# Optimization experiments

Measured on AMD Instinct MI355X. Metric: run time of the kernel, lower is better.

Reference implementation:

```python
import jax, jax.numpy as jnp
import numpy as np
from jax import lax

B, C, H, W = 8, 128, 128, 128
HEADS = 16
HEAD_C = C // HEADS  # 8
SLOPE = 0.2
EPS = 1e-12


def _conv(x, w, b, padding, groups=1):
    # x: [B,C,H,W], w: [O,I/groups,kh,kw]
    y = lax.conv_general_dilated(
        x, w, window_strides=(1, 1), padding=padding,
        dimension_numbers=("NCHW", "OIHW", "NCHW"),
        feature_group_count=groups)
    return y + b[None, :, None, None]


def _conv_block(x, conv1_w, conv1_b, conv2_w, conv2_b, dw_w, dw_b, sc_w, sc_b):
    h = _conv(x, conv1_w, conv1_b, ((1, 1), (1, 1)))            # 3x3, zero pad
    h = jnp.where(h >= 0, h, SLOPE * h)                          # LeakyReLU
    h = _conv(h, conv2_w, conv2_b, ((0, 0), (0, 0)))             # 1x1
    hp = jnp.pad(h, ((0, 0), (0, 0), (1, 1), (1, 1)), mode="reflect")
    h = _conv(hp, dw_w, dw_b, ((0, 0), (0, 0)), groups=C)        # depthwise 3x3, reflect pad
    h = jnp.where(h >= 0, h, SLOPE * h)
    sc = _conv(x, sc_w, sc_b, ((0, 0), (0, 0)))                  # 1x1 shortcut
    return h + sc


def setup_inputs() -> dict:
    key = jax.random.key(0)
    ks = jax.random.split(key, 10)
    s = 0.05
    return {
        "x1": jax.random.normal(ks[0], (B, C, H, W), jnp.float32),
        "x2": jax.random.normal(ks[1], (B, C, H, W), jnp.float32),
        "temperature": jnp.ones((HEADS, 1, 1), jnp.float32),
        "conv1_w": jax.random.normal(ks[2], (C, C, 3, 3), jnp.float32) * s,
        "conv1_b": jnp.zeros((C,), jnp.float32),
        "conv2_w": jax.random.normal(ks[3], (C, C, 1, 1), jnp.float32) * s,
        "conv2_b": jnp.zeros((C,), jnp.float32),
        "dw_w": jax.random.normal(ks[4], (C, 1, 3, 3), jnp.float32) * s,
        "dw_b": jnp.zeros((C,), jnp.float32),
        "sc_w": jax.random.normal(ks[5], (C, C, 1, 1), jnp.float32) * s,
        "sc_b": jnp.zeros((C,), jnp.float32),
    }


def reference(x1, x2, temperature, conv1_w, conv1_b, conv2_w, conv2_b,
              dw_w, dw_b, sc_w, sc_b):
    b, c, h, w = x2.shape
    # b (head c) h w -> b head c (h w)
    qk = x1.reshape(b, HEADS, HEAD_C, h * w)
    v = x2.reshape(b, HEADS, HEAD_C, h * w)
    # L2-normalize over spatial dim (F.normalize, eps=1e-12)
    norm = jnp.sqrt(jnp.sum(qk * qk, axis=-1, keepdims=True))
    qn = qk / jnp.maximum(norm, EPS)
    # channel attention: [b, head, c, c]
    attn = jnp.einsum("bhcn,bhdn->bhcd", qn, qn) * temperature
    attn = jax.nn.softmax(attn, axis=-1)
    out = jnp.einsum("bhcd,bhdn->bhcn", attn, v)
    out = out.reshape(b, c, h, w)
    out = _conv_block(out, conv1_w, conv1_b, conv2_w, conv2_b,
                      dw_w, dw_b, sc_w, sc_b)
    return out + x1
```

## Files before the change

### kernel.cpp

```cpp
#include <hip/hip_runtime.h>
#include <hip/hip_bf16.h>

typedef __attribute__((ext_vector_type(8))) short short8;
typedef __attribute__((ext_vector_type(4))) float f32x4;

#define NB 8
#define NC 128
#define NHW 128
#define NSP (NHW*NHW)
#define SLOPE 0.2f
#define EPSN 1e-12f
#define PADW 130

static __device__ __forceinline__ unsigned short f2bf(float f) {
    __hip_bfloat16 h = __float2bfloat16(f);
    return *reinterpret_cast<unsigned short*>(&h);
}
static __device__ __forceinline__ float bf2f(__hip_bfloat16 h) {
    return __bfloat162float(h);
}

__global__ void prep_all(const float* __restrict__ c1w, const float* __restrict__ c2w,
                         const float* __restrict__ scw,
                         __hip_bfloat16* __restrict__ wb1, __hip_bfloat16* __restrict__ wb2,
                         __hip_bfloat16* __restrict__ wbsc, __hip_bfloat16* __restrict__ yt2) {
    int idx = blockIdx.x * 256 + threadIdx.x;
    if (idx < 147456) {
        int kw = idx % 3; int t = idx / 3;
        int kh = t % 3;   t /= 3;
        int i  = t % 128; int o = t / 128;
        int tap = kh * 3 + kw;
        int half = i >> 6, icc = (i >> 5) & 1, lk = (i >> 3) & 3, j = i & 7;
        int wn = o >> 6, c = (o >> 4) & 3, l15 = o & 15;
        int lane = lk * 16 + l15;
        size_t chunk = (size_t)tap * 32 + half * 16 + wn * 8 + icc * 4 + c;
        wb1[chunk * 512 + lane * 8 + j] = __float2bfloat16(c1w[idx]);
    } else if (idx < 180224) {
        int i2 = idx - 147456;
        const float* src = (i2 < 16384) ? c2w : scw;
        __hip_bfloat16* dst = (i2 < 16384) ? wb2 : wbsc;
        int e = i2 & 16383;
        int i = e & 127, o = e >> 7;
        int kk = i >> 5, lk = (i >> 3) & 3, j = i & 7;
        int wn = o >> 6, c = (o >> 4) & 3, l15 = o & 15;
        int lane = lk * 16 + l15;
        size_t chunk = ((size_t)(wn * 4 + kk) * 4 + c);
        dst[chunk * 512 + lane * 8 + j] = __float2bfloat16(src[e]);
    } else if (idx < 184352) {
        int t = idx - 180224;
        int b = t / 516, s = t % 516;
        int row, col;
        if (s < 130)      { row = 0;           col = s; }
        else if (s < 260) { row = 129;         col = s - 130; }
        else if (s < 388) { row = s - 260 + 1; col = 0; }
        else              { row = s - 388 + 1; col = 129; }
        uint4* dst = reinterpret_cast<uint4*>(yt2 + ((size_t)(b * PADW + row) * PADW + col) * 128);
        uint4 z = make_uint4(0u, 0u, 0u, 0u);
#pragma unroll
        for (int i = 0; i < 16; ++i) dst[i] = z;
    }
}

__global__ __launch_bounds__(256) void gram_part(const float* __restrict__ x1,
                                                 float* __restrict__ Gp) {
    int bh = blockIdx.x & 127;
    int q  = blockIdx.x >> 7;
    const float* base = x1 + (size_t)bh * 8 * NSP + q * 4096;
    float acc[8][8];
#pragma unroll
    for (int c = 0; c < 8; c++)
#pragma unroll
        for (int d = 0; d < 8; d++) acc[c][d] = 0.f;

    for (int n = threadIdx.x; n < 4096; n += 256) {
        float v[8];
#pragma unroll
        for (int c = 0; c < 8; c++) v[c] = base[c * NSP + n];
#pragma unroll
        for (int c = 0; c < 8; c++)
#pragma unroll
            for (int d = 0; d < 8; d++)
                acc[c][d] = fmaf(v[c], v[d], acc[c][d]);
    }
#pragma unroll
    for (int c = 0; c < 8; c++)
#pragma unroll
        for (int d = 0; d < 8; d++)
            for (int off = 32; off > 0; off >>= 1)
                acc[c][d] += __shfl_down(acc[c][d], off);

    __shared__ float red[4][64];
    int wv = threadIdx.x >> 6;
    if ((threadIdx.x & 63) == 0) {
#pragma unroll
        for (int c = 0; c < 8; c++)
#pragma unroll
            for (int d = 0; d < 8; d++) red[wv][c * 8 + d] = acc[c][d];
    }
    __syncthreads();
    if (threadIdx.x < 64)
        Gp[(size_t)(q * 128 + bh) * 64 + threadIdx.x] =
            red[0][threadIdx.x] + red[1][threadIdx.x] + red[2][threadIdx.x] + red[3][threadIdx.x];
}

__global__ void softmax_kernel(const float* __restrict__ Gp, const float* __restrict__ temp,
                               float* __restrict__ attn) {
    int bh = blockIdx.x; int hd = bh & 15;
    int t = threadIdx.x;
    float g = 0.f;
#pragma unroll
    for (int q = 0; q < 4; q++) g += Gp[(size_t)(q * 128 + bh) * 64 + t];
    __shared__ float gs[64];
    gs[t] = g;
    __syncthreads();
    int c = t >> 3, d = t & 7;
    float nc = fmaxf(sqrtf(gs[c * 8 + c]), EPSN);
    float nd = fmaxf(sqrtf(gs[d * 8 + d]), EPSN);
    float a = g / (nc * nd) * temp[hd];
    float m = a;
#pragma unroll
    for (int off = 4; off > 0; off >>= 1) m = fmaxf(m, __shfl_xor(m, off));
    float e = __expf(a - m);
    float s = e;
#pragma unroll
    for (int off = 4; off > 0; off >>= 1) s += __shfl_xor(s, off);
    attn[bh * 64 + t] = e / s;
}

__global__ __launch_bounds__(256) void av_v3(const float* __restrict__ x2,
                                             const float* __restrict__ attn,
                                             __hip_bfloat16* __restrict__ yt2) {
    int b  = blockIdx.x >> 8;
    int p0 = (blockIdx.x & 255) << 6;
    __shared__ float vt[128][65];
    __shared__ float at[16][65];
    for (int idx = threadIdx.x; idx < 1024; idx += 256)
        at[idx >> 6][idx & 63] = attn[(size_t)b * 1024 + idx];
    for (int idx = threadIdx.x; idx < 8192; idx += 256) {
        int row = idx >> 6, col = idx & 63;
        vt[row][col] = x2[(size_t)(b * 128 + row) * NSP + p0 + col];
    }
    __syncthreads();
    for (int idx = threadIdx.x; idx < 1024; idx += 256) {
        int cq = idx & 15;
        int p  = idx >> 4;
        float vv[8];
#pragma unroll
        for (int d = 0; d < 8; d++) vv[d] = vt[cq * 8 + d][p];
        unsigned int pk[4];
#pragma unroll
        for (int c = 0; c < 8; c += 2) {
            float s0 = 0.f, s1 = 0.f;
#pragma unroll
            for (int d = 0; d < 8; d++) {
                s0 = fmaf(at[cq][c * 8 + d], vv[d], s0);
                s1 = fmaf(at[cq][(c + 1) * 8 + d], vv[d], s1);
            }
            pk[c >> 1] = (unsigned int)f2bf(s0) | ((unsigned int)f2bf(s1) << 16);
        }
        uint4 st; st.x = pk[0]; st.y = pk[1]; st.z = pk[2]; st.w = pk[3];
        int n = p0 + p;
        int hh = n >> 7, wc = n & 127;
        *reinterpret_cast<uint4*>(
            yt2 + ((size_t)(b * PADW + hh + 1) * PADW + wc + 1) * 128 + cq * 8) = st;
    }
}

#define BPTR(s) (wf1 + ((size_t)(((((s) % 18) >> 1) * 32) + ((s) / 18) * 16 + wn * 8 + ((s) & 1) * 4)) * 64 + lane)

__global__ __launch_bounds__(256, 4) void fused_conv(const __hip_bfloat16* __restrict__ yt2,
                                                     const __hip_bfloat16* __restrict__ wb1,
                                                     const __hip_bfloat16* __restrict__ wb2,
                                                     const __hip_bfloat16* __restrict__ wbsc,
                                                     const float* __restrict__ b1,
                                                     const float* __restrict__ b2,
                                                     const float* __restrict__ bsc,
                                                     __hip_bfloat16* __restrict__ h2,
                                                     __hip_bfloat16* __restrict__ scp) {
    __shared__ uint4 smem[1584];
    char* smem_raw = (char*)smem;
    int bid = blockIdx.x;
    int swz = (bid & 7) * 256 + (bid >> 3);
    int b = swz >> 8;
    int rh = swz & 255;
    int h = rh >> 1;
    int p0 = (rh & 1) * 64;
    int tid = threadIdx.x;
    int lane = tid & 63;
    int wid = tid >> 6;
    int wm = wid >> 1, wn = wid & 1;
    int l15 = lane & 15;
    int lk = lane >> 4;

    const short8* wf1  = reinterpret_cast<const short8*>(wb1);
    const short8* wf2  = reinterpret_cast<const short8*>(wb2);
    const short8* wfsc = reinterpret_cast<const short8*>(wbsc);

    f32x4 acc[2][4];
#pragma unroll
    for (int a = 0; a < 2; a++)
#pragma unroll
        for (int c = 0; c < 4; c++) acc[a][c] = (f32x4){0.f, 0.f, 0.f, 0.f};

    const short8* wpi = BPTR(0);
    short8 bA0 = wpi[0], bA1 = wpi[64], bA2 = wpi[128], bA3 = wpi[192];
    wpi = BPTR(1);
    short8 bB0 = wpi[0], bB1 = wpi[64], bB2 = wpi[128], bB3 = wpi[192];

#pragma unroll
    for (int half = 0; half < 2; ++half) {
        __syncthreads();
        for (int idx = tid; idx < 1584; idx += 256) {
            int g = idx & 7;
            int colr = idx >> 3;
            int col = colr % 66;
            int r = colr / 66;
            uint4 v = *reinterpret_cast<const uint4*>(
                yt2 + ((size_t)(b * PADW + h + r) * PADW + (p0 + col)) * 128 + half * 64 + g * 8);
            smem[(r * 66 + col) * 8 + (g ^ (col & 7))] = v;
        }
        __syncthreads();

#pragma unroll
        for (int gp = 0; gp < 9; ++gp) {
            const int kh = gp / 3, kw = gp - kh * 3;
            {
                const int s = half * 18 + gp * 2;
                short8 n0, n1, n2, n3;
                const bool more = (s + 2 < 36);
                if (more) {
                    const short8* w2 = BPTR(s + 2);
                    n0 = w2[0]; n1 = w2[64]; n2 = w2[128]; n3 = w2[192];
                }
                short8 afr[2];
#pragma unroll
                for (int a = 0; a < 2; ++a) {
                    int col = (wm * 2 + a) * 16 + l15 + kw;
                    int g = lk;
                    afr[a] = *reinterpret_cast<const short8*>(
                        &smem[(kh * 66 + col) * 8 + (g ^ (col & 7))]);
                }
                __builtin_amdgcn_s_setprio(1);
#pragma unroll
                for (int a = 0; a < 2; ++a) {
                    acc[a][0] = __builtin_amdgcn_mfma_f32_16x16x32_bf16(afr[a], bA0, acc[a][0], 0, 0, 0);
                    acc[a][1] = __builtin_amdgcn_mfma_f32_16x16x32_bf16(afr[a], bA1, acc[a][1], 0, 0, 0);
                    acc[a][2] = __builtin_amdgcn_mfma_f32_16x16x32_bf16(afr[a], bA2, acc[a][2], 0, 0, 0);
                    acc[a][3] = __builtin_amdgcn_mfma_f32_16x16x32_bf16(afr[a], bA3, acc[a][3], 0, 0, 0);
                }
                __builtin_amdgcn_s_setprio(0);
                if (more) { bA0 = n0; bA1 = n1; bA2 = n2; bA3 = n3; }
            }
            {
                const int s = half * 18 + gp * 2 + 1;
                short8 n0, n1, n2, n3;
                const bool more = (s + 2 < 36);
                if (more) {
                    const short8* w2 = BPTR(s + 2);
                    n0 = w2[0]; n1 = w2[64]; n2 = w2[128]; n3 = w2[192];
                }
                short8 afr[2];
#pragma unroll
                for (int a = 0; a < 2; ++a) {
                    int col = (wm * 2 + a) * 16 + l15 + kw;
                    int g = 4 + lk;
                    afr[a] = *reinterpret_cast<const short8*>(
                        &smem[(kh * 66 + col) * 8 + (g ^ (col & 7))]);
                }
                __builtin_amdgcn_s_setprio(1);
#pragma unroll
                for (int a = 0; a < 2; ++a) {
                    acc[a][0] = __builtin_amdgcn_mfma_f32_16x16x32_bf16(afr[a], bB0, acc[a][0], 0, 0, 0);
                    acc[a][1] = __builtin_amdgcn_mfma_f32_16x16x32_bf16(afr[a], bB1, acc[a][1], 0, 0, 0);
                    acc[a][2] = __builtin_amdgcn_mfma_f32_16x16x32_bf16(afr[a], bB2, acc[a][2], 0, 0, 0);
                    acc[a][3] = __builtin_amdgcn_mfma_f32_16x16x32_bf16(afr[a], bB3, acc[a][3], 0, 0, 0);
                }
                __builtin_amdgcn_s_setprio(0);
                if (more) { bB0 = n0; bB1 = n1; bB2 = n2; bB3 = n3; }
            }
        }
    }

    __syncthreads();
#pragma unroll
    for (int c = 0; c < 4; ++c) {
        int o = wn * 64 + c * 16 + l15;
        float bv = b1[o];
        int go = o >> 3, ob = (o & 7) << 1;
#pragma unroll
        for (int a = 0; a < 2; ++a) {
            int pb = (wm * 2 + a) * 16 + lk * 4;
#pragma unroll
            for (int j = 0; j < 4; ++j) {
                int p = pb + j;
                float v = acc[a][c][j] + bv;
                v = v >= 0.f ? v : SLOPE * v;
                *reinterpret_cast<__hip_bfloat16*>(
                    smem_raw + p * 256 + (((go ^ (p & 15)) << 4) | ob)) = __float2bfloat16(v);
            }
        }
    }
    __syncthreads();

#pragma unroll
    for (int a = 0; a < 2; a++)
#pragma unroll
        for (int c = 0; c < 4; c++) acc[a][c] = (f32x4){0.f, 0.f, 0.f, 0.f};
#pragma unroll
    for (int kk = 0; kk < 4; ++kk) {
        short8 bfr[4];
#pragma unroll
        for (int c = 0; c < 4; ++c)
            bfr[c] = wf2[((size_t)(wn * 4 + kk) * 4 + c) * 64 + lane];
        short8 afr[2];
        int g = kk * 4 + lk;
#pragma unroll
        for (int a = 0; a < 2; ++a) {
            int p = (wm * 2 + a) * 16 + l15;
            afr[a] = *reinterpret_cast<const short8*>(smem_raw + p * 256 + ((g ^ (p & 15)) << 4));
        }
        __builtin_amdgcn_s_setprio(1);
#pragma unroll
        for (int a = 0; a < 2; ++a)
#pragma unroll
            for (int c = 0; c < 4; ++c)
                acc[a][c] = __builtin_amdgcn_mfma_f32_16x16x32_bf16(afr[a], bfr[c], acc[a][c], 0, 0, 0);
        __builtin_amdgcn_s_setprio(0);
    }
#pragma unroll
    for (int c = 0; c < 4; ++c) {
        int o = wn * 64 + c * 16 + l15;
        float bv = b2[o];
        size_t obase = ((size_t)(b * 128 + o) * 128 + h) * 128 + p0;
#pragma unroll
        for (int a = 0; a < 2; ++a) {
            int w0 = (wm * 2 + a) * 16 + lk * 4;
            uint2 st;
            st.x = (unsigned int)f2bf(acc[a][c][0] + bv) | ((unsigned int)f2bf(acc[a][c][1] + bv) << 16);
            st.y = (unsigned int)f2bf(acc[a][c][2] + bv) | ((unsigned int)f2bf(acc[a][c][3] + bv) << 16);
            *reinterpret_cast<uint2*>(h2 + obase + w0) = st;
        }
    }

    __syncthreads();
    for (int idx = tid; idx < 1024; idx += 256) {
        int p = idx >> 4, g = idx & 15;
        uint4 v = *reinterpret_cast<const uint4*>(
            yt2 + ((size_t)(b * PADW + h + 1) * PADW + (p0 + 1 + p)) * 128 + g * 8);
        *reinterpret_cast<uint4*>(smem_raw + p * 256 + ((g ^ (p & 15)) << 4)) = v;
    }
    __syncthreads();

#pragma unroll
    for (int a = 0; a < 2; a++)
#pragma unroll
        for (int c = 0; c < 4; c++) acc[a][c] = (f32x4){0.f, 0.f, 0.f, 0.f};
#pragma unroll
    for (int kk = 0; kk < 4; ++kk) {
        short8 bfr[4];
#pragma unroll
        for (int c = 0; c < 4; ++c)
            bfr[c] = wfsc[((size_t)(wn * 4 + kk) * 4 + c) * 64 + lane];
        short8 afr[2];
        int g = kk * 4 + lk;
#pragma unroll
        for (int a = 0; a < 2; ++a) {
            int p = (wm * 2 + a) * 16 + l15;
            afr[a] = *reinterpret_cast<const short8*>(smem_raw + p * 256 + ((g ^ (p & 15)) << 4));
        }
        __builtin_amdgcn_s_setprio(1);
#pragma unroll
        for (int a = 0; a < 2; ++a)
#pragma unroll
            for (int c = 0; c < 4; ++c)
                acc[a][c] = __builtin_amdgcn_mfma_f32_16x16x32_bf16(afr[a], bfr[c], acc[a][c], 0, 0, 0);
        __builtin_amdgcn_s_setprio(0);
    }
#pragma unroll
    for (int c = 0; c < 4; ++c) {
        int o = wn * 64 + c * 16 + l15;
        float bv = bsc[o];
        size_t obase = ((size_t)(b * 128 + o) * 128 + h) * 128 + p0;
#pragma unroll
        for (int a = 0; a < 2; ++a) {
            int w0 = (wm * 2 + a) * 16 + lk * 4;
            uint2 st;
            st.x = (unsigned int)f2bf(acc[a][c][0] + bv) | ((unsigned int)f2bf(acc[a][c][1] + bv) << 16);
            st.y = (unsigned int)f2bf(acc[a][c][2] + bv) | ((unsigned int)f2bf(acc[a][c][3] + bv) << 16);
            *reinterpret_cast<uint2*>(scp + obase + w0) = st;
        }
    }
}

__global__ __launch_bounds__(256) void dw_v3(const __hip_bfloat16* __restrict__ h2,
                                             const __hip_bfloat16* __restrict__ scp,
                                             const float* __restrict__ x1,
                                             const float* __restrict__ dww,
                                             const float* __restrict__ dwb,
                                             float* __restrict__ out) {
    int bid = blockIdx.x;
    int swz = (bid & 7) * 1024 + (bid >> 3);
    size_t tidx = (size_t)swz * 256 + threadIdx.x;
    int w0 = (int)((tidx & 15) << 3);
    int hh = (int)((tidx >> 4) & 127);
    int bc = (int)(tidx >> 11);
    int c  = bc & 127;
    const __hip_bfloat16* src = h2 + ((size_t)bc << 14);
    float wg[9];
#pragma unroll
    for (int k = 0; k < 9; ++k) wg[k] = dww[c * 9 + k];
    float bv = dwb[c];
    float a8[8];
#pragma unroll
    for (int j = 0; j < 8; ++j) a8[j] = bv;
#pragma unroll
    for (int kh = 0; kh < 3; ++kh) {
        int ih = hh + kh - 1;
        ih = ih < 0 ? 1 : (ih > 127 ? 126 : ih);
        const __hip_bfloat16* row = src + ih * 128;
        short8 mid = *reinterpret_cast<const short8*>(row + w0);
        float v[10];
        v[0] = bf2f(row[w0 == 0 ? 1 : w0 - 1]);
#pragma unroll
        for (int j = 0; j < 8; ++j)
            v[j + 1] = __uint_as_float((unsigned int)(unsigned short)mid[j] << 16);
        v[9] = bf2f(row[w0 == 120 ? 126 : w0 + 8]);
#pragma unroll
        for (int kw = 0; kw < 3; ++kw)
#pragma unroll
            for (int j = 0; j < 8; ++j)
                a8[j] = fmaf(v[j + kw], wg[kh * 3 + kw], a8[j]);
    }
    size_t ob = ((size_t)bc << 14) + hh * 128 + w0;
    short8 sv = *reinterpret_cast<const short8*>(scp + ob);
    float4 xa = *reinterpret_cast<const float4*>(x1 + ob);
    float4 xb = *reinterpret_cast<const float4*>(x1 + ob + 4);
#pragma unroll
    for (int j = 0; j < 8; ++j) a8[j] = a8[j] >= 0.f ? a8[j] : SLOPE * a8[j];
    float4 o0, o1;
    o0.x = xa.x + __uint_as_float((unsigned int)(unsigned short)sv[0] << 16) + a8[0];
    o0.y = xa.y + __uint_as_float((unsigned int)(unsigned short)sv[1] << 16) + a8[1];
    o0.z = xa.z + __uint_as_float((unsigned int)(unsigned short)sv[2] << 16) + a8[2];
    o0.w = xa.w + __uint_as_float((unsigned int)(unsigned short)sv[3] << 16) + a8[3];
    o1.x = xb.x + __uint_as_float((unsigned int)(unsigned short)sv[4] << 16) + a8[4];
    o1.y = xb.y + __uint_as_float((unsigned int)(unsigned short)sv[5] << 16) + a8[5];
    o1.z = xb.z + __uint_as_float((unsigned int)(unsigned short)sv[6] << 16) + a8[6];
    o1.w = xb.w + __uint_as_float((unsigned int)(unsigned short)sv[7] << 16) + a8[7];
    *reinterpret_cast<float4*>(out + ob) = o0;
    *reinterpret_cast<float4*>(out + ob + 4) = o1;
}

extern "C" void kernel_launch(void* const* d_in, const int* in_sizes, int n_in,
                              void* d_out, int out_size, void* d_ws, size_t ws_size,
                              hipStream_t stream) {
    const float* x1   = (const float*)d_in[0];
    const float* x2   = (const float*)d_in[1];
    const float* temp = (const float*)d_in[2];
    const float* c1w  = (const float*)d_in[3];
    const float* c1b  = (const float*)d_in[4];
    const float* c2w  = (const float*)d_in[5];
    const float* c2b  = (const float*)d_in[6];
    const float* dww  = (const float*)d_in[7];
    const float* dwb  = (const float*)d_in[8];
    const float* scw  = (const float*)d_in[9];
    const float* scb  = (const float*)d_in[10];
    float* out = (float*)d_out;
    char* ws = (char*)d_ws;

    float*          attn = (float*)(ws + (32 << 10));
    float*          Gp   = (float*)(ws + (64 << 10));
    __hip_bfloat16* wb1  = (__hip_bfloat16*)(ws + (192 << 10));
    __hip_bfloat16* wb2  = (__hip_bfloat16*)(ws + (480 << 10));
    __hip_bfloat16* wbsc = (__hip_bfloat16*)(ws + (512 << 10));
    __hip_bfloat16* yt2  = (__hip_bfloat16*)(ws + ((size_t)1 << 20));
    __hip_bfloat16* h2b  = (__hip_bfloat16*)(ws + ((size_t)36 << 20));
    __hip_bfloat16* scp  = (__hip_bfloat16*)(ws + ((size_t)68 << 20));

    prep_all<<<721, 256, 0, stream>>>(c1w, c2w, scw, wb1, wb2, wbsc, yt2);

    gram_part<<<512, 256, 0, stream>>>(x1, Gp);
    softmax_kernel<<<128, 64, 0, stream>>>(Gp, temp, attn);
    av_v3<<<2048, 256, 0, stream>>>(x2, attn, yt2);

    fused_conv<<<2048, 256, 0, stream>>>(yt2, wb1, wb2, wbsc, c1b, c2b, scb, h2b, scp);
    dw_v3<<<8192, 256, 0, stream>>>(h2b, scp, x1, dww, dwb, out);
}
```

Measured before the change: 162.6 us.

## Process two output rows per block in fused conv to reuse weights and halo

Each fused_conv block now computes two image rows by 64 columns (128 pixels) instead of one row, and the grid halves to 1024 blocks. The input tile grows to four padded rows, so halo loads per output row drop and each weight fragment fetched from global memory feeds twice as many MFMAs. Accumulators double to 4x4 per wave, which raises register pressure, and launch bounds are lowered to 3 blocks per CU to allow this at the cost of occupancy.

```diff
diff --git a/kernel.cpp b/kernel.cpp
--- a/kernel.cpp
+++ b/kernel.cpp
@@ -168,7 +168,7 @@
 
 #define BPTR(s) (wf1 + ((size_t)(((((s) % 18) >> 1) * 32) + ((s) / 18) * 16 + wn * 8 + ((s) & 1) * 4)) * 64 + lane)
 
-__global__ __launch_bounds__(256, 4) void fused_conv(const __hip_bfloat16* __restrict__ yt2,
+__global__ __launch_bounds__(256, 3) void fused_conv(const __hip_bfloat16* __restrict__ yt2,
                                                      const __hip_bfloat16* __restrict__ wb1,
                                                      const __hip_bfloat16* __restrict__ wb2,
                                                      const __hip_bfloat16* __restrict__ wbsc,
@@ -177,14 +177,14 @@
                                                      const float* __restrict__ bsc,
                                                      __hip_bfloat16* __restrict__ h2,
                                                      __hip_bfloat16* __restrict__ scp) {
-    __shared__ uint4 smem[1584];
+    __shared__ uint4 smem[2112];
     char* smem_raw = (char*)smem;
     int bid = blockIdx.x;
-    int swz = (bid & 7) * 256 + (bid >> 3);
-    int b = swz >> 8;
-    int rh = swz & 255;
-    int h = rh >> 1;
-    int p0 = (rh & 1) * 64;
+    int swz = (bid & 7) * 128 + (bid >> 3);
+    int b = swz >> 7;
+    int rp = swz & 127;
+    int h0 = (rp >> 1) << 1;
+    int p0 = (rp & 1) * 64;
     int tid = threadIdx.x;
     int lane = tid & 63;
     int wid = tid >> 6;
@@ -196,9 +196,9 @@
     const short8* wf2  = reinterpret_cast<const short8*>(wb2);
     const short8* wfsc = reinterpret_cast<const short8*>(wbsc);
 
-    f32x4 acc[2][4];
-#pragma unroll
-    for (int a = 0; a < 2; a++)
+    f32x4 acc[4][4];
+#pragma unroll
+    for (int a = 0; a < 4; a++)
 #pragma unroll
         for (int c = 0; c < 4; c++) acc[a][c] = (f32x4){0.f, 0.f, 0.f, 0.f};
 
@@ -210,13 +210,13 @@
 #pragma unroll
     for (int half = 0; half < 2; ++half) {
         __syncthreads();
-        for (int idx = tid; idx < 1584; idx += 256) {
+        for (int idx = tid; idx < 2112; idx += 256) {
             int g = idx & 7;
             int colr = idx >> 3;
             int col = colr % 66;
             int r = colr / 66;
             uint4 v = *reinterpret_cast<const uint4*>(
-                yt2 + ((size_t)(b * PADW + h + r) * PADW + (p0 + col)) * 128 + half * 64 + g * 8);
+                yt2 + ((size_t)(b * PADW + h0 + r) * PADW + (p0 + col)) * 128 + half * 64 + g * 8);
             smem[(r * 66 + col) * 8 + (g ^ (col & 7))] = v;
         }
         __syncthreads();
@@ -232,17 +232,17 @@
                     const short8* w2 = BPTR(s + 2);
                     n0 = w2[0]; n1 = w2[64]; n2 = w2[128]; n3 = w2[192];
                 }
-                short8 afr[2];
-#pragma unroll
-                for (int a = 0; a < 2; ++a) {
-                    int col = (wm * 2 + a) * 16 + l15 + kw;
+                short8 afr[4];
+#pragma unroll
+                for (int a = 0; a < 4; ++a) {
+                    int col = a * 16 + l15 + kw;
                     int g = lk;
                     afr[a] = *reinterpret_cast<const short8*>(
-                        &smem[(kh * 66 + col) * 8 + (g ^ (col & 7))]);
+                        &smem[((wm + kh) * 66 + col) * 8 + (g ^ (col & 7))]);
                 }
                 __builtin_amdgcn_s_setprio(1);
 #pragma unroll
-                for (int a = 0; a < 2; ++a) {
+                for (int a = 0; a < 4; ++a) {
                     acc[a][0] = __builtin_amdgcn_mfma_f32_16x16x32_bf16(afr[a], bA0, acc[a][0], 0, 0, 0);
                     acc[a][1] = __builtin_amdgcn_mfma_f32_16x16x32_bf16(afr[a], bA1, acc[a][1], 0, 0, 0);
                     acc[a][2] = __builtin_amdgcn_mfma_f32_16x16x32_bf16(afr[a], bA2, acc[a][2], 0, 0, 0);
@@ -259,17 +259,17 @@
                     const short8* w2 = BPTR(s + 2);
                     n0 = w2[0]; n1 = w2[64]; n2 = w2[128]; n3 = w2[192];
                 }
-                short8 afr[2];
-#pragma unroll
-                for (int a = 0; a < 2; ++a) {
-                    int col = (wm * 2 + a) * 16 + l15 + kw;
+                short8 afr[4];
+#pragma unroll
+                for (int a = 0; a < 4; ++a) {
+                    int col = a * 16 + l15 + kw;
                     int g = 4 + lk;
                     afr[a] = *reinterpret_cast<const short8*>(
-                        &smem[(kh * 66 + col) * 8 + (g ^ (col & 7))]);
+                        &smem[((wm + kh) * 66 + col) * 8 + (g ^ (col & 7))]);
                 }
                 __builtin_amdgcn_s_setprio(1);
 #pragma unroll
-                for (int a = 0; a < 2; ++a) {
+                for (int a = 0; a < 4; ++a) {
                     acc[a][0] = __builtin_amdgcn_mfma_f32_16x16x32_bf16(afr[a], bB0, acc[a][0], 0, 0, 0);
                     acc[a][1] = __builtin_amdgcn_mfma_f32_16x16x32_bf16(afr[a], bB1, acc[a][1], 0, 0, 0);
                     acc[a][2] = __builtin_amdgcn_mfma_f32_16x16x32_bf16(afr[a], bB2, acc[a][2], 0, 0, 0);
@@ -288,8 +288,8 @@
         float bv = b1[o];
         int go = o >> 3, ob = (o & 7) << 1;
 #pragma unroll
-        for (int a = 0; a < 2; ++a) {
-            int pb = (wm * 2 + a) * 16 + lk * 4;
+        for (int a = 0; a < 4; ++a) {
+            int pb = wm * 64 + a * 16 + lk * 4;
 #pragma unroll
             for (int j = 0; j < 4; ++j) {
                 int p = pb + j;
@@ -303,7 +303,7 @@
     __syncthreads();
 
 #pragma unroll
-    for (int a = 0; a < 2; a++)
+    for (int a = 0; a < 4; a++)
 #pragma unroll
         for (int c = 0; c < 4; c++) acc[a][c] = (f32x4){0.f, 0.f, 0.f, 0.f};
 #pragma unroll
@@ -312,16 +312,16 @@
 #pragma unroll
         for (int c = 0; c < 4; ++c)
             bfr[c] = wf2[((size_t)(wn * 4 + kk) * 4 + c) * 64 + lane];
-        short8 afr[2];
+        short8 afr[4];
         int g = kk * 4 + lk;
 #pragma unroll
-        for (int a = 0; a < 2; ++a) {
-            int p = (wm * 2 + a) * 16 + l15;
+        for (int a = 0; a < 4; ++a) {
+            int p = (wm * 4 + a) * 16 + l15;
             afr[a] = *reinterpret_cast<const short8*>(smem_raw + p * 256 + ((g ^ (p & 15)) << 4));
         }
         __builtin_amdgcn_s_setprio(1);
 #pragma unroll
-        for (int a = 0; a < 2; ++a)
+        for (int a = 0; a < 4; ++a)
 #pragma unroll
             for (int c = 0; c < 4; ++c)
                 acc[a][c] = __builtin_amdgcn_mfma_f32_16x16x32_bf16(afr[a], bfr[c], acc[a][c], 0, 0, 0);
@@ -331,28 +331,28 @@
     for (int c = 0; c < 4; ++c) {
         int o = wn * 64 + c * 16 + l15;
         float bv = b2[o];
-        size_t obase = ((size_t)(b * 128 + o) * 128 + h) * 128 + p0;
-#pragma unroll
-        for (int a = 0; a < 2; ++a) {
-            int w0 = (wm * 2 + a) * 16 + lk * 4;
+#pragma unroll
+        for (int a = 0; a < 4; ++a) {
+            int p2 = (wm * 4 + a) * 16 + lk * 4;
+            size_t obase = ((size_t)(b * 128 + o) * 128 + h0 + (p2 >> 6)) * 128 + p0 + (p2 & 63);
             uint2 st;
             st.x = (unsigned int)f2bf(acc[a][c][0] + bv) | ((unsigned int)f2bf(acc[a][c][1] + bv) << 16);
             st.y = (unsigned int)f2bf(acc[a][c][2] + bv) | ((unsigned int)f2bf(acc[a][c][3] + bv) << 16);
-            *reinterpret_cast<uint2*>(h2 + obase + w0) = st;
-        }
-    }
-
-    __syncthreads();
-    for (int idx = tid; idx < 1024; idx += 256) {
+            *reinterpret_cast<uint2*>(h2 + obase) = st;
+        }
+    }
+
+    __syncthreads();
+    for (int idx = tid; idx < 2048; idx += 256) {
         int p = idx >> 4, g = idx & 15;
         uint4 v = *reinterpret_cast<const uint4*>(
-            yt2 + ((size_t)(b * PADW + h + 1) * PADW + (p0 + 1 + p)) * 128 + g * 8);
+            yt2 + ((size_t)(b * PADW + h0 + (p >> 6) + 1) * PADW + (p0 + (p & 63) + 1)) * 128 + g * 8);
         *reinterpret_cast<uint4*>(smem_raw + p * 256 + ((g ^ (p & 15)) << 4)) = v;
     }
     __syncthreads();
 
 #pragma unroll
-    for (int a = 0; a < 2; a++)
+    for (int a = 0; a < 4; a++)
 #pragma unroll
         for (int c = 0; c < 4; c++) acc[a][c] = (f32x4){0.f, 0.f, 0.f, 0.f};
 #pragma unroll
@@ -361,16 +361,16 @@
 #pragma unroll
         for (int c = 0; c < 4; ++c)
             bfr[c] = wfsc[((size_t)(wn * 4 + kk) * 4 + c) * 64 + lane];
-        short8 afr[2];
+        short8 afr[4];
         int g = kk * 4 + lk;
 #pragma unroll
-        for (int a = 0; a < 2; ++a) {
-            int p = (wm * 2 + a) * 16 + l15;
+        for (int a = 0; a < 4; ++a) {
+            int p = (wm * 4 + a) * 16 + l15;
             afr[a] = *reinterpret_cast<const short8*>(smem_raw + p * 256 + ((g ^ (p & 15)) << 4));
         }
         __builtin_amdgcn_s_setprio(1);
 #pragma unroll
-        for (int a = 0; a < 2; ++a)
+        for (int a = 0; a < 4; ++a)
 #pragma unroll
             for (int c = 0; c < 4; ++c)
                 acc[a][c] = __builtin_amdgcn_mfma_f32_16x16x32_bf16(afr[a], bfr[c], acc[a][c], 0, 0, 0);
@@ -380,14 +380,14 @@
     for (int c = 0; c < 4; ++c) {
         int o = wn * 64 + c * 16 + l15;
         float bv = bsc[o];
-        size_t obase = ((size_t)(b * 128 + o) * 128 + h) * 128 + p0;
-#pragma unroll
-        for (int a = 0; a < 2; ++a) {
-            int w0 = (wm * 2 + a) * 16 + lk * 4;
+#pragma unroll
+        for (int a = 0; a < 4; ++a) {
+            int p2 = (wm * 4 + a) * 16 + lk * 4;
+            size_t obase = ((size_t)(b * 128 + o) * 128 + h0 + (p2 >> 6)) * 128 + p0 + (p2 & 63);
             uint2 st;
             st.x = (unsigned int)f2bf(acc[a][c][0] + bv) | ((unsigned int)f2bf(acc[a][c][1] + bv) << 16);
             st.y = (unsigned int)f2bf(acc[a][c][2] + bv) | ((unsigned int)f2bf(acc[a][c][3] + bv) << 16);
-            *reinterpret_cast<uint2*>(scp + obase + w0) = st;
+            *reinterpret_cast<uint2*>(scp + obase) = st;
         }
     }
 }
@@ -482,6 +482,6 @@
     softmax_kernel<<<128, 64, 0, stream>>>(Gp, temp, attn);
     av_v3<<<2048, 256, 0, stream>>>(x2, attn, yt2);
 
-    fused_conv<<<2048, 256, 0, stream>>>(yt2, wb1, wb2, wbsc, c1b, c2b, scb, h2b, scp);
+    fused_conv<<<1024, 256, 0, stream>>>(yt2, wb1, wb2, wbsc, c1b, c2b, scb, h2b, scp);
     dw_v3<<<8192, 256, 0, stream>>>(h2b, scp, x1, dww, dwb, out);
 }
```

New measurement: 189.3 us. +16.4%, slower.

## Fuse 1x1 shortcut GEMM into center tap of 3x3 conv loop

Applied to the files above, without the earlier changes.

The 1x1 shortcut convolution previously reloaded the center row of the input into shared memory and ran its own GEMM pass after the 1x1 conv2 stage. It now reuses the A fragments already loaded for the center tap (gp==4) of the 3x3 conv and accumulates into a second set of accumulators, writing the shortcut output early. This removes a global-to-LDS reload, two barriers and a separate loop. The cost is extra accumulator registers, so launch bounds drop the occupancy hint from 4 to 3 waves per SIMD.

```diff
diff --git a/kernel.cpp b/kernel.cpp
--- a/kernel.cpp
+++ b/kernel.cpp
@@ -168,7 +168,7 @@
 
 #define BPTR(s) (wf1 + ((size_t)(((((s) % 18) >> 1) * 32) + ((s) / 18) * 16 + wn * 8 + ((s) & 1) * 4)) * 64 + lane)
 
-__global__ __launch_bounds__(256, 4) void fused_conv(const __hip_bfloat16* __restrict__ yt2,
+__global__ __launch_bounds__(256, 3) void fused_conv(const __hip_bfloat16* __restrict__ yt2,
                                                      const __hip_bfloat16* __restrict__ wb1,
                                                      const __hip_bfloat16* __restrict__ wb2,
                                                      const __hip_bfloat16* __restrict__ wbsc,
@@ -197,10 +197,14 @@
     const short8* wfsc = reinterpret_cast<const short8*>(wbsc);
 
     f32x4 acc[2][4];
+    f32x4 accS[2][4];
 #pragma unroll
     for (int a = 0; a < 2; a++)
 #pragma unroll
-        for (int c = 0; c < 4; c++) acc[a][c] = (f32x4){0.f, 0.f, 0.f, 0.f};
+        for (int c = 0; c < 4; c++) {
+            acc[a][c] = (f32x4){0.f, 0.f, 0.f, 0.f};
+            accS[a][c] = (f32x4){0.f, 0.f, 0.f, 0.f};
+        }
 
     const short8* wpi = BPTR(0);
     short8 bA0 = wpi[0], bA1 = wpi[64], bA2 = wpi[128], bA3 = wpi[192];
@@ -249,6 +253,20 @@
                     acc[a][3] = __builtin_amdgcn_mfma_f32_16x16x32_bf16(afr[a], bA3, acc[a][3], 0, 0, 0);
                 }
                 __builtin_amdgcn_s_setprio(0);
+                if (gp == 4) {
+                    const int kk = half * 2;
+                    short8 s0 = wfsc[((size_t)(wn * 4 + kk) * 4 + 0) * 64 + lane];
+                    short8 s1 = wfsc[((size_t)(wn * 4 + kk) * 4 + 1) * 64 + lane];
+                    short8 s2 = wfsc[((size_t)(wn * 4 + kk) * 4 + 2) * 64 + lane];
+                    short8 s3 = wfsc[((size_t)(wn * 4 + kk) * 4 + 3) * 64 + lane];
+#pragma unroll
+                    for (int a = 0; a < 2; ++a) {
+                        accS[a][0] = __builtin_amdgcn_mfma_f32_16x16x32_bf16(afr[a], s0, accS[a][0], 0, 0, 0);
+                        accS[a][1] = __builtin_amdgcn_mfma_f32_16x16x32_bf16(afr[a], s1, accS[a][1], 0, 0, 0);
+                        accS[a][2] = __builtin_amdgcn_mfma_f32_16x16x32_bf16(afr[a], s2, accS[a][2], 0, 0, 0);
+                        accS[a][3] = __builtin_amdgcn_mfma_f32_16x16x32_bf16(afr[a], s3, accS[a][3], 0, 0, 0);
+                    }
+                }
                 if (more) { bA0 = n0; bA1 = n1; bA2 = n2; bA3 = n3; }
             }
             {
@@ -276,8 +294,37 @@
                     acc[a][3] = __builtin_amdgcn_mfma_f32_16x16x32_bf16(afr[a], bB3, acc[a][3], 0, 0, 0);
                 }
                 __builtin_amdgcn_s_setprio(0);
+                if (gp == 4) {
+                    const int kk = half * 2 + 1;
+                    short8 s0 = wfsc[((size_t)(wn * 4 + kk) * 4 + 0) * 64 + lane];
+                    short8 s1 = wfsc[((size_t)(wn * 4 + kk) * 4 + 1) * 64 + lane];
+                    short8 s2 = wfsc[((size_t)(wn * 4 + kk) * 4 + 2) * 64 + lane];
+                    short8 s3 = wfsc[((size_t)(wn * 4 + kk) * 4 + 3) * 64 + lane];
+#pragma unroll
+                    for (int a = 0; a < 2; ++a) {
+                        accS[a][0] = __builtin_amdgcn_mfma_f32_16x16x32_bf16(afr[a], s0, accS[a][0], 0, 0, 0);
+                        accS[a][1] = __builtin_amdgcn_mfma_f32_16x16x32_bf16(afr[a], s1, accS[a][1], 0, 0, 0);
+                        accS[a][2] = __builtin_amdgcn_mfma_f32_16x16x32_bf16(afr[a], s2, accS[a][2], 0, 0, 0);
+                        accS[a][3] = __builtin_amdgcn_mfma_f32_16x16x32_bf16(afr[a], s3, accS[a][3], 0, 0, 0);
+                    }
+                }
                 if (more) { bB0 = n0; bB1 = n1; bB2 = n2; bB3 = n3; }
             }
+        }
+    }
+
+#pragma unroll
+    for (int c = 0; c < 4; ++c) {
+        int o = wn * 64 + c * 16 + l15;
+        float bv = bsc[o];
+        size_t obase = ((size_t)(b * 128 + o) * 128 + h) * 128 + p0;
+#pragma unroll
+        for (int a = 0; a < 2; ++a) {
+            int w0 = (wm * 2 + a) * 16 + lk * 4;
+            uint2 st;
+            st.x = (unsigned int)f2bf(accS[a][c][0] + bv) | ((unsigned int)f2bf(accS[a][c][1] + bv) << 16);
+            st.y = (unsigned int)f2bf(accS[a][c][2] + bv) | ((unsigned int)f2bf(accS[a][c][3] + bv) << 16);
+            *reinterpret_cast<uint2*>(scp + obase + w0) = st;
         }
     }
 
@@ -339,55 +386,6 @@
             st.x = (unsigned int)f2bf(acc[a][c][0] + bv) | ((unsigned int)f2bf(acc[a][c][1] + bv) << 16);
             st.y = (unsigned int)f2bf(acc[a][c][2] + bv) | ((unsigned int)f2bf(acc[a][c][3] + bv) << 16);
             *reinterpret_cast<uint2*>(h2 + obase + w0) = st;
-        }
-    }
-
-    __syncthreads();
-    for (int idx = tid; idx < 1024; idx += 256) {
-        int p = idx >> 4, g = idx & 15;
-        uint4 v = *reinterpret_cast<const uint4*>(
-            yt2 + ((size_t)(b * PADW + h + 1) * PADW + (p0 + 1 + p)) * 128 + g * 8);
-        *reinterpret_cast<uint4*>(smem_raw + p * 256 + ((g ^ (p & 15)) << 4)) = v;
-    }
-    __syncthreads();
-
-#pragma unroll
-    for (int a = 0; a < 2; a++)
-#pragma unroll
-        for (int c = 0; c < 4; c++) acc[a][c] = (f32x4){0.f, 0.f, 0.f, 0.f};
-#pragma unroll
-    for (int kk = 0; kk < 4; ++kk) {
-        short8 bfr[4];
-#pragma unroll
-        for (int c = 0; c < 4; ++c)
-            bfr[c] = wfsc[((size_t)(wn * 4 + kk) * 4 + c) * 64 + lane];
-        short8 afr[2];
-        int g = kk * 4 + lk;
-#pragma unroll
-        for (int a = 0; a < 2; ++a) {
-            int p = (wm * 2 + a) * 16 + l15;
-            afr[a] = *reinterpret_cast<const short8*>(smem_raw + p * 256 + ((g ^ (p & 15)) << 4));
-        }
-        __builtin_amdgcn_s_setprio(1);
-#pragma unroll
-        for (int a = 0; a < 2; ++a)
-#pragma unroll
-            for (int c = 0; c < 4; ++c)
-                acc[a][c] = __builtin_amdgcn_mfma_f32_16x16x32_bf16(afr[a], bfr[c], acc[a][c], 0, 0, 0);
-        __builtin_amdgcn_s_setprio(0);
-    }
-#pragma unroll
-    for (int c = 0; c < 4; ++c) {
-        int o = wn * 64 + c * 16 + l15;
-        float bv = bsc[o];
-        size_t obase = ((size_t)(b * 128 + o) * 128 + h) * 128 + p0;
-#pragma unroll
-        for (int a = 0; a < 2; ++a) {
-            int w0 = (wm * 2 + a) * 16 + lk * 4;
-            uint2 st;
-            st.x = (unsigned int)f2bf(acc[a][c][0] + bv) | ((unsigned int)f2bf(acc[a][c][1] + bv) << 16);
-            st.y = (unsigned int)f2bf(acc[a][c][2] + bv) | ((unsigned int)f2bf(acc[a][c][3] + bv) << 16);
-            *reinterpret_cast<uint2*>(scp + obase + w0) = st;
         }
     }
 }
```

Measured after the change: 164.7 us. About the same (+1.3%).
